# Performance work log

Measured on AMD Instinct MI355X. Metric: run time of the kernel, lower is better.

## Reference

```python
import jax, jax.numpy as jnp
import numpy as np

TOP_K = 2


def setup_inputs() -> dict:
    key = jax.random.key(0)
    k1, k2 = jax.random.split(key)
    N, D, E = 16384, 2048, 64
    x = jax.random.normal(k1, (N, D), dtype=jnp.float32)
    W = jax.random.normal(k2, (E, D), dtype=jnp.float32) * (1.0 / np.sqrt(D))
    return {"x": x, "W": W}


def reference(x, W):
    # x: (N, d_model), W: (n_experts, d_model) -> logits (N, n_experts)
    logits = jnp.einsum('nd,ed->ne', x, W)
    router_probs = jax.nn.softmax(logits, axis=-1)
    top_k_weights, top_k_indices = jax.lax.top_k(router_probs, TOP_K)
    top_k_weights = top_k_weights / (jnp.sum(top_k_weights, axis=-1, keepdims=True) + 1e-9)
    return (router_probs, top_k_indices, top_k_weights)
```

## Files before the change

### kernel.cpp

```cpp
#include <hip/hip_runtime.h>
#include <math.h>

typedef _Float16 f16x8 __attribute__((ext_vector_type(8)));
typedef _Float16 f16x4 __attribute__((ext_vector_type(4)));
typedef float    f32x16 __attribute__((ext_vector_type(16)));

constexpr int D_DIM = 2048;
constexpr int N_EXP = 64;
constexpr int BM    = 32;
constexpr int KW    = 512;
constexpr int KC    = 32;
constexpr int NCH   = KW / KC;
constexpr int XST   = 40;
constexpr int PWB   = 15360;

__global__ __launch_bounds__(256, 2) void topk_router_kernel(
    const float* __restrict__ x, const float* __restrict__ Wm,
    float* __restrict__ outProbs, float* __restrict__ outIdx,
    float* __restrict__ outWt)
{
    __shared__ __align__(16) char LDSB[4 * PWB];

    const int t    = threadIdx.x;
    const int lane = t & 63;
    const int wave = t >> 6;
    const int rowBase = blockIdx.x * BM;

    char* base = LDSB + wave * PWB;
    _Float16 (*X1)[XST] = (_Float16(*)[XST])(base);
    _Float16 (*X2)[XST] = (_Float16(*)[XST])(base + 2560);
    _Float16 (*W1)[XST] = (_Float16(*)[XST])(base + 5120);
    _Float16 (*W2)[XST] = (_Float16(*)[XST])(base + 10240);

    const int k0   = wave * KW;
    const int srow = lane >> 3;
    const int sc4  = (lane & 7) * 4;

    const float* xg = x  + (size_t)(rowBase + srow) * D_DIM + k0 + sc4;
    const float* wg = Wm + (size_t)srow * D_DIM + k0 + sc4;

    float4 px[4], pw[8];
#pragma unroll
    for (int f = 0; f < 4; ++f) px[f] = *(const float4*)(xg + (size_t)(8 * f) * D_DIM);
#pragma unroll
    for (int f = 0; f < 8; ++f) pw[f] = *(const float4*)(wg + (size_t)(8 * f) * D_DIM);

    f32x16 acc0[2], acc1[2];
#pragma unroll
    for (int n = 0; n < 2; ++n)
#pragma unroll
        for (int i = 0; i < 16; ++i) { acc0[n][i] = 0.f; acc1[n][i] = 0.f; }

    const int fr = lane & 31;
    const int fg = (lane >> 5) * 8;

    for (int ch = 0; ch < NCH; ++ch) {
#pragma unroll
        for (int f = 0; f < 4; ++f) {
            const int r = srow + 8 * f;
            f16x4 h1, h2;
            h1[0] = (_Float16)px[f].x; h1[1] = (_Float16)px[f].y;
            h1[2] = (_Float16)px[f].z; h1[3] = (_Float16)px[f].w;
            h2[0] = (_Float16)((px[f].x - (float)h1[0]) * 2048.f);
            h2[1] = (_Float16)((px[f].y - (float)h1[1]) * 2048.f);
            h2[2] = (_Float16)((px[f].z - (float)h1[2]) * 2048.f);
            h2[3] = (_Float16)((px[f].w - (float)h1[3]) * 2048.f);
            *(f16x4*)&X1[r][sc4] = h1;
            *(f16x4*)&X2[r][sc4] = h2;
        }
#pragma unroll
        for (int f = 0; f < 8; ++f) {
            const int e = srow + 8 * f;
            f16x4 h1, h2;
            h1[0] = (_Float16)pw[f].x; h1[1] = (_Float16)pw[f].y;
            h1[2] = (_Float16)pw[f].z; h1[3] = (_Float16)pw[f].w;
            h2[0] = (_Float16)((pw[f].x - (float)h1[0]) * 2048.f);
            h2[1] = (_Float16)((pw[f].y - (float)h1[1]) * 2048.f);
            h2[2] = (_Float16)((pw[f].z - (float)h1[2]) * 2048.f);
            h2[3] = (_Float16)((pw[f].w - (float)h1[3]) * 2048.f);
            *(f16x4*)&W1[e][sc4] = h1;
            *(f16x4*)&W2[e][sc4] = h2;
        }

        if (ch + 1 < NCH) {
            const int kb = (ch + 1) * KC;
#pragma unroll
            for (int f = 0; f < 4; ++f)
                px[f] = *(const float4*)(xg + (size_t)(8 * f) * D_DIM + kb);
#pragma unroll
            for (int f = 0; f < 8; ++f)
                pw[f] = *(const float4*)(wg + (size_t)(8 * f) * D_DIM + kb);
        }

#pragma unroll
        for (int ks = 0; ks < 2; ++ks) {
            const int ko = ks * 16 + fg;
            const f16x8 A1 = *(const f16x8*)&X1[fr][ko];
            const f16x8 A2 = *(const f16x8*)&X2[fr][ko];
#pragma unroll
            for (int n = 0; n < 2; ++n) {
                const f16x8 B1 = *(const f16x8*)&W1[n * 32 + fr][ko];
                const f16x8 B2 = *(const f16x8*)&W2[n * 32 + fr][ko];
                acc0[n] = __builtin_amdgcn_mfma_f32_32x32x16_f16(A1, B1, acc0[n], 0, 0, 0);
                acc1[n] = __builtin_amdgcn_mfma_f32_32x32x16_f16(A1, B2, acc1[n], 0, 0, 0);
                acc1[n] = __builtin_amdgcn_mfma_f32_32x32x16_f16(A2, B1, acc1[n], 0, 0, 0);
            }
        }
    }

    float* scr = (float*)base;
    const float S2 = 1.0f / 2048.0f;
#pragma unroll
    for (int n = 0; n < 2; ++n)
#pragma unroll
        for (int rg = 0; rg < 16; ++rg) {
            const int row = (rg & 3) + 8 * (rg >> 2) + 4 * (lane >> 5);
            const int col = n * 32 + fr;
            scr[row * 68 + col] = acc0[n][rg] + acc1[n][rg] * S2;
        }
    __syncthreads();

    const int r  = t >> 3;
    const int e0 = (t & 7) * 8;
    float lg[8];
#pragma unroll
    for (int j = 0; j < 8; ++j) lg[j] = 0.f;
#pragma unroll
    for (int w = 0; w < 4; ++w) {
        const float* s = (const float*)(LDSB + w * PWB) + r * 68 + e0;
        const float4 a = *(const float4*)s;
        const float4 b = *(const float4*)(s + 4);
        lg[0] += a.x; lg[1] += a.y; lg[2] += a.z; lg[3] += a.w;
        lg[4] += b.x; lg[5] += b.y; lg[6] += b.z; lg[7] += b.w;
    }

    float v1 = lg[0]; int i1 = e0; float v2 = -INFINITY; int i2 = 0;
#pragma unroll
    for (int j = 1; j < 8; ++j) {
        const float v = lg[j]; const int id = e0 + j;
        if (v > v1)      { v2 = v1; i2 = i1; v1 = v; i1 = id; }
        else if (v > v2) { v2 = v;  i2 = id; }
    }
#pragma unroll
    for (int m = 1; m < 8; m <<= 1) {
        const float ov1 = __shfl_xor(v1, m, 64); const int oi1 = __shfl_xor(i1, m, 64);
        const float ov2 = __shfl_xor(v2, m, 64); const int oi2 = __shfl_xor(i2, m, 64);
        float n1, n2; int ni1, ni2;
        const bool o1_wins = (ov1 > v1) || (ov1 == v1 && oi1 < i1);
        if (o1_wins) {
            n1 = ov1; ni1 = oi1;
            const bool a1_beats_o2 = (v1 > ov2) || (v1 == ov2 && i1 < oi2);
            if (a1_beats_o2) { n2 = v1;  ni2 = i1;  } else { n2 = ov2; ni2 = oi2; }
        } else {
            n1 = v1; ni1 = i1;
            const bool o1_beats_a2 = (ov1 > v2) || (ov1 == v2 && oi1 < i2);
            if (o1_beats_a2) { n2 = ov1; ni2 = oi1; } else { n2 = v2;  ni2 = i2;  }
        }
        v1 = n1; i1 = ni1; v2 = n2; i2 = ni2;
    }

    float ee[8]; float S = 0.f;
#pragma unroll
    for (int j = 0; j < 8; ++j) { ee[j] = __expf(lg[j] - v1); S += ee[j]; }
    S += __shfl_xor(S, 1, 64);
    S += __shfl_xor(S, 2, 64);
    S += __shfl_xor(S, 4, 64);
    const float rS = 1.0f / S;

    const int row = rowBase + r;
    float4 pa = {ee[0] * rS, ee[1] * rS, ee[2] * rS, ee[3] * rS};
    float4 pb = {ee[4] * rS, ee[5] * rS, ee[6] * rS, ee[7] * rS};
    *(float4*)(outProbs + (size_t)row * N_EXP + e0)     = pa;
    *(float4*)(outProbs + (size_t)row * N_EXP + e0 + 4) = pb;

    if ((t & 7) == 0) {
        const float p1 = rS;
        const float p2 = __expf(v2 - v1) * rS;
        const float den = p1 + p2 + 1e-9f;
        outIdx[row * 2 + 0] = (float)i1;
        outIdx[row * 2 + 1] = (float)i2;
        outWt [row * 2 + 0] = p1 / den;
        outWt [row * 2 + 1] = p2 / den;
    }
}

extern "C" void kernel_launch(void* const* d_in, const int* in_sizes, int n_in,
                              void* d_out, int out_size, void* d_ws, size_t ws_size,
                              hipStream_t stream) {
    const float* x = (const float*)d_in[0];
    const float* W = (const float*)d_in[1];
    const int nRows = in_sizes[0] / D_DIM;

    float* outProbs = (float*)d_out;
    float* outIdx   = outProbs + (size_t)nRows * N_EXP;
    float* outWt    = outIdx   + (size_t)nRows * 2;

    dim3 grid(nRows / BM), block(256);
    topk_router_kernel<<<grid, block, 0, stream>>>(x, W, outProbs, outIdx, outWt);
}
```

Before: 196.0 us.

## Pre-split W into fp16 halves and load MFMA operands directly from global

Adds a small pre-kernel that splits W into high and low fp16 parts in workspace once per call, so the main kernel no longer converts W in every block. The main kernel drops the LDS staging of X and W and loads MFMA operand fragments straight from global memory into registers, with a two-deep register double buffer and the x split done in registers. This removes LDS writes and reads plus the per-block W conversion, at the cost of an extra kernel launch, more registers, and less coalesced per-lane global loads.

```diff
diff --git a/kernel.cpp b/kernel.cpp
--- a/kernel.cpp
+++ b/kernel.cpp
@@ -2,7 +2,6 @@
 #include <math.h>
 
 typedef _Float16 f16x8 __attribute__((ext_vector_type(8)));
-typedef _Float16 f16x4 __attribute__((ext_vector_type(4)));
 typedef float    f32x16 __attribute__((ext_vector_type(16)));
 
 constexpr int D_DIM = 2048;
@@ -11,39 +10,77 @@
 constexpr int KW    = 512;
 constexpr int KC    = 32;
 constexpr int NCH   = KW / KC;
-constexpr int XST   = 40;
-constexpr int PWB   = 15360;
+
+__global__ __launch_bounds__(256) void split_w_kernel(
+    const float* __restrict__ W, _Float16* __restrict__ W1, _Float16* __restrict__ W2)
+{
+    const int i = (blockIdx.x * 256 + threadIdx.x) * 8;
+    const float4 a = *(const float4*)(W + i);
+    const float4 b = *(const float4*)(W + i + 4);
+    const float v[8] = {a.x, a.y, a.z, a.w, b.x, b.y, b.z, b.w};
+    f16x8 h1, h2;
+#pragma unroll
+    for (int j = 0; j < 8; ++j) {
+        const _Float16 p = (_Float16)v[j];
+        h1[j] = p;
+        h2[j] = (_Float16)((v[j] - (float)p) * 2048.f);
+    }
+    *(f16x8*)(W1 + i) = h1;
+    *(f16x8*)(W2 + i) = h2;
+}
+
+__device__ inline void split8(const float4& a, const float4& b, f16x8& h1, f16x8& h2)
+{
+    const float v[8] = {a.x, a.y, a.z, a.w, b.x, b.y, b.z, b.w};
+#pragma unroll
+    for (int j = 0; j < 8; ++j) {
+        const _Float16 p = (_Float16)v[j];
+        h1[j] = p;
+        h2[j] = (_Float16)((v[j] - (float)p) * 2048.f);
+    }
+}
 
 __global__ __launch_bounds__(256, 2) void topk_router_kernel(
-    const float* __restrict__ x, const float* __restrict__ Wm,
+    const float* __restrict__ x, const _Float16* __restrict__ W1,
+    const _Float16* __restrict__ W2,
     float* __restrict__ outProbs, float* __restrict__ outIdx,
     float* __restrict__ outWt)
 {
-    __shared__ __align__(16) char LDSB[4 * PWB];
+    __shared__ __align__(16) float scratch[4][BM * 68];
 
     const int t    = threadIdx.x;
     const int lane = t & 63;
     const int wave = t >> 6;
     const int rowBase = blockIdx.x * BM;
 
-    char* base = LDSB + wave * PWB;
-    _Float16 (*X1)[XST] = (_Float16(*)[XST])(base);
-    _Float16 (*X2)[XST] = (_Float16(*)[XST])(base + 2560);
-    _Float16 (*W1)[XST] = (_Float16(*)[XST])(base + 5120);
-    _Float16 (*W2)[XST] = (_Float16(*)[XST])(base + 10240);
-
-    const int k0   = wave * KW;
-    const int srow = lane >> 3;
-    const int sc4  = (lane & 7) * 4;
-
-    const float* xg = x  + (size_t)(rowBase + srow) * D_DIM + k0 + sc4;
-    const float* wg = Wm + (size_t)srow * D_DIM + k0 + sc4;
-
-    float4 px[4], pw[8];
-#pragma unroll
-    for (int f = 0; f < 4; ++f) px[f] = *(const float4*)(xg + (size_t)(8 * f) * D_DIM);
-#pragma unroll
-    for (int f = 0; f < 8; ++f) pw[f] = *(const float4*)(wg + (size_t)(8 * f) * D_DIM);
+    const int fr = lane & 31;
+    const int fh = (lane >> 5) * 8;
+
+    const int k0 = wave * KW;
+    const float*    xp  = x  + (size_t)(rowBase + fr) * D_DIM + k0 + fh;
+    const _Float16* w1a = W1 + (size_t)fr        * D_DIM + k0 + fh;
+    const _Float16* w1b = W1 + (size_t)(32 + fr) * D_DIM + k0 + fh;
+    const _Float16* w2a = W2 + (size_t)fr        * D_DIM + k0 + fh;
+    const _Float16* w2b = W2 + (size_t)(32 + fr) * D_DIM + k0 + fh;
+
+    float4 xA[2][4];
+    f16x8  wA[2][8];
+
+#define LOADC(b, ch) do {                                   \
+        const int kb_ = (ch) * KC;                          \
+        xA[b][0] = *(const float4*)(xp + kb_);              \
+        xA[b][1] = *(const float4*)(xp + kb_ + 4);          \
+        xA[b][2] = *(const float4*)(xp + kb_ + 16);         \
+        xA[b][3] = *(const float4*)(xp + kb_ + 20);         \
+        wA[b][0] = *(const f16x8*)(w1a + kb_);              \
+        wA[b][1] = *(const f16x8*)(w2a + kb_);              \
+        wA[b][2] = *(const f16x8*)(w1b + kb_);              \
+        wA[b][3] = *(const f16x8*)(w2b + kb_);              \
+        wA[b][4] = *(const f16x8*)(w1a + kb_ + 16);         \
+        wA[b][5] = *(const f16x8*)(w2a + kb_ + 16);         \
+        wA[b][6] = *(const f16x8*)(w1b + kb_ + 16);         \
+        wA[b][7] = *(const f16x8*)(w2b + kb_ + 16);         \
+    } while (0)
 
     f32x16 acc0[2], acc1[2];
 #pragma unroll
@@ -51,64 +88,32 @@
 #pragma unroll
         for (int i = 0; i < 16; ++i) { acc0[n][i] = 0.f; acc1[n][i] = 0.f; }
 
-    const int fr = lane & 31;
-    const int fg = (lane >> 5) * 8;
-
+    LOADC(0, 0);
+    LOADC(1, 1);
+
+#pragma unroll
     for (int ch = 0; ch < NCH; ++ch) {
-#pragma unroll
-        for (int f = 0; f < 4; ++f) {
-            const int r = srow + 8 * f;
-            f16x4 h1, h2;
-            h1[0] = (_Float16)px[f].x; h1[1] = (_Float16)px[f].y;
-            h1[2] = (_Float16)px[f].z; h1[3] = (_Float16)px[f].w;
-            h2[0] = (_Float16)((px[f].x - (float)h1[0]) * 2048.f);
-            h2[1] = (_Float16)((px[f].y - (float)h1[1]) * 2048.f);
-            h2[2] = (_Float16)((px[f].z - (float)h1[2]) * 2048.f);
-            h2[3] = (_Float16)((px[f].w - (float)h1[3]) * 2048.f);
-            *(f16x4*)&X1[r][sc4] = h1;
-            *(f16x4*)&X2[r][sc4] = h2;
+        const int b = ch & 1;
+#pragma unroll
+        for (int ks = 0; ks < 2; ++ks) {
+            f16x8 A1, A2;
+            split8(xA[b][ks * 2], xA[b][ks * 2 + 1], A1, A2);
+            const f16x8 B1a = wA[b][ks * 4 + 0];
+            const f16x8 B2a = wA[b][ks * 4 + 1];
+            const f16x8 B1b = wA[b][ks * 4 + 2];
+            const f16x8 B2b = wA[b][ks * 4 + 3];
+            acc0[0] = __builtin_amdgcn_mfma_f32_32x32x16_f16(A1, B1a, acc0[0], 0, 0, 0);
+            acc1[0] = __builtin_amdgcn_mfma_f32_32x32x16_f16(A1, B2a, acc1[0], 0, 0, 0);
+            acc1[0] = __builtin_amdgcn_mfma_f32_32x32x16_f16(A2, B1a, acc1[0], 0, 0, 0);
+            acc0[1] = __builtin_amdgcn_mfma_f32_32x32x16_f16(A1, B1b, acc0[1], 0, 0, 0);
+            acc1[1] = __builtin_amdgcn_mfma_f32_32x32x16_f16(A1, B2b, acc1[1], 0, 0, 0);
+            acc1[1] = __builtin_amdgcn_mfma_f32_32x32x16_f16(A2, B1b, acc1[1], 0, 0, 0);
         }
-#pragma unroll
-        for (int f = 0; f < 8; ++f) {
-            const int e = srow + 8 * f;
-            f16x4 h1, h2;
-            h1[0] = (_Float16)pw[f].x; h1[1] = (_Float16)pw[f].y;
-            h1[2] = (_Float16)pw[f].z; h1[3] = (_Float16)pw[f].w;
-            h2[0] = (_Float16)((pw[f].x - (float)h1[0]) * 2048.f);
-            h2[1] = (_Float16)((pw[f].y - (float)h1[1]) * 2048.f);
-            h2[2] = (_Float16)((pw[f].z - (float)h1[2]) * 2048.f);
-            h2[3] = (_Float16)((pw[f].w - (float)h1[3]) * 2048.f);
-            *(f16x4*)&W1[e][sc4] = h1;
-            *(f16x4*)&W2[e][sc4] = h2;
-        }
-
-        if (ch + 1 < NCH) {
-            const int kb = (ch + 1) * KC;
-#pragma unroll
-            for (int f = 0; f < 4; ++f)
-                px[f] = *(const float4*)(xg + (size_t)(8 * f) * D_DIM + kb);
-#pragma unroll
-            for (int f = 0; f < 8; ++f)
-                pw[f] = *(const float4*)(wg + (size_t)(8 * f) * D_DIM + kb);
-        }
-
-#pragma unroll
-        for (int ks = 0; ks < 2; ++ks) {
-            const int ko = ks * 16 + fg;
-            const f16x8 A1 = *(const f16x8*)&X1[fr][ko];
-            const f16x8 A2 = *(const f16x8*)&X2[fr][ko];
-#pragma unroll
-            for (int n = 0; n < 2; ++n) {
-                const f16x8 B1 = *(const f16x8*)&W1[n * 32 + fr][ko];
-                const f16x8 B2 = *(const f16x8*)&W2[n * 32 + fr][ko];
-                acc0[n] = __builtin_amdgcn_mfma_f32_32x32x16_f16(A1, B1, acc0[n], 0, 0, 0);
-                acc1[n] = __builtin_amdgcn_mfma_f32_32x32x16_f16(A1, B2, acc1[n], 0, 0, 0);
-                acc1[n] = __builtin_amdgcn_mfma_f32_32x32x16_f16(A2, B1, acc1[n], 0, 0, 0);
-            }
-        }
-    }
-
-    float* scr = (float*)base;
+        if (ch + 2 < NCH) LOADC(b, ch + 2);
+    }
+#undef LOADC
+
+    float* scr = scratch[wave];
     const float S2 = 1.0f / 2048.0f;
 #pragma unroll
     for (int n = 0; n < 2; ++n)
@@ -127,7 +132,7 @@
     for (int j = 0; j < 8; ++j) lg[j] = 0.f;
 #pragma unroll
     for (int w = 0; w < 4; ++w) {
-        const float* s = (const float*)(LDSB + w * PWB) + r * 68 + e0;
+        const float* s = scratch[w] + r * 68 + e0;
         const float4 a = *(const float4*)s;
         const float4 b = *(const float4*)(s + 4);
         lg[0] += a.x; lg[1] += a.y; lg[2] += a.z; lg[3] += a.w;
@@ -195,6 +200,10 @@
     float* outIdx   = outProbs + (size_t)nRows * N_EXP;
     float* outWt    = outIdx   + (size_t)nRows * 2;
 
-    dim3 grid(nRows / BM), block(256);
-    topk_router_kernel<<<grid, block, 0, stream>>>(x, W, outProbs, outIdx, outWt);
-}
+    _Float16* W1h = (_Float16*)d_ws;
+    _Float16* W2h = W1h + (size_t)N_EXP * D_DIM;
+
+    split_w_kernel<<<dim3(64), dim3(256), 0, stream>>>(W, W1h, W2h);
+    topk_router_kernel<<<dim3(nRows / BM), dim3(256), 0, stream>>>(
+        x, W1h, W2h, outProbs, outIdx, outWt);
+}
```

After: 223.8 us. 1.14x slower.
